# Performance work log

Measured on AMD Instinct MI355X. Metric: run time of the kernel, lower is better.

## Reference

```python
import jax, jax.numpy as jnp
import numpy as np

B, N, C = 2048, 128, 128
H = 4
NW = 64


def setup_inputs() -> dict:
    key = jax.random.key(0)
    ks = jax.random.split(key, 6)
    return {
        "x": jax.random.normal(ks[0], (B, N, C), dtype=jnp.float32),
        "mask": jax.random.normal(ks[1], (NW, N, N), dtype=jnp.float32),
        "qkv_w": jax.random.normal(ks[2], (3 * C, C), dtype=jnp.float32) * (C ** -0.5),
        "qkv_b": jax.random.normal(ks[3], (3 * C,), dtype=jnp.float32) * 0.02,
        "proj_w": jax.random.normal(ks[4], (C, C), dtype=jnp.float32) * (C ** -0.5),
        "proj_b": jax.random.normal(ks[5], (C,), dtype=jnp.float32) * 0.02,
    }


def reference(x, mask, qkv_w, qkv_b, proj_w, proj_b):
    b, n, c = x.shape
    h = H
    hd = c // h
    scale = hd ** -0.5
    # qkv projection: [B,N,3C] -> [3,B,H,N,hd]
    qkv = (x @ qkv_w.T + qkv_b).reshape(b, n, 3, h, hd).transpose(2, 0, 3, 1, 4)
    q, k, v = qkv[0], qkv[1], qkv[2]
    # scores [B,H,N,N]
    attn = jnp.einsum("bhnd,bhmd->bhnm", q, k) * scale
    nw = mask.shape[0]
    # add per-window mask: view as [B//nW, nW, H, N, N] + mask[None,:,None]
    attn = attn.reshape(b // nw, nw, h, n, n) + mask[None, :, None, :, :]
    attn = attn.reshape(b, h, n, n)
    attn = jax.nn.softmax(attn, axis=-1)
    out = jnp.einsum("bhnm,bhmd->bhnd", attn, v)
    out = out.transpose(0, 2, 1, 3).reshape(b, n, c)
    out = out @ proj_w.T + proj_b
    return out
```

## Files before the change

kernel.cpp:

```cpp
#include <hip/hip_runtime.h>

typedef __bf16 bf16x8 __attribute__((ext_vector_type(8)));
typedef __bf16 bf16x4 __attribute__((ext_vector_type(4)));
typedef float  f32x4  __attribute__((ext_vector_type(4)));

#define LDS_XO 0
#define LDS_Q  32768
#define LDS_K  65536
#define LDS_VT 98304
#define LDS_P  131072
#define LDS_TOTAL 147456

__device__ __forceinline__ int swz(int row, int colb) {
    return row * 256 + (colb ^ ((row & 7) << 4));
}
__device__ __forceinline__ int pswz(int row, int colb) {
    return row * 128 + (colb ^ ((row & 7) << 4));
}

__global__ void prep_weights(const float* __restrict__ qkv_w,
                             const float* __restrict__ proj_w,
                             __bf16* __restrict__ wq, __bf16* __restrict__ wp) {
    int i = blockIdx.x * 256 + threadIdx.x;
    wq[i] = (__bf16)qkv_w[i];
    if (i < 16384) wp[i] = (__bf16)proj_w[i];
}

__global__ void __launch_bounds__(512, 2)
attn_fused(const float* __restrict__ x, const float* __restrict__ mask,
           const float* __restrict__ qkv_b, const float* __restrict__ proj_b,
           const __bf16* __restrict__ wq, const __bf16* __restrict__ wp,
           float* __restrict__ out) {
    extern __shared__ char smem[];
    const int b    = blockIdx.x;
    const int tid  = threadIdx.x;
    const int wave = tid >> 6;
    const int lane = tid & 63;
    const int l16  = lane & 15;
    const int lg   = lane >> 4;

    {
        const float* xb = x + (size_t)b * 16384;
        #pragma unroll
        for (int it = 0; it < 4; ++it) {
            int i   = it * 512 + tid;
            int row = i >> 4;
            int c8  = (i & 15) << 3;
            float4 f0 = *(const float4*)(xb + row * 128 + c8);
            float4 f1 = *(const float4*)(xb + row * 128 + c8 + 4);
            bf16x8 v;
            v[0] = (__bf16)f0.x; v[1] = (__bf16)f0.y; v[2] = (__bf16)f0.z; v[3] = (__bf16)f0.w;
            v[4] = (__bf16)f1.x; v[5] = (__bf16)f1.y; v[6] = (__bf16)f1.z; v[7] = (__bf16)f1.w;
            *(bf16x8*)(smem + LDS_XO + swz(row, c8 * 2)) = v;
        }
    }
    __syncthreads();

    const int j0 = wave * 48;
    #pragma unroll
    for (int pass = 0; pass < 2; ++pass) {
        f32x4 acc[3][4];
        #pragma unroll
        for (int jt = 0; jt < 3; ++jt)
            #pragma unroll
            for (int nt = 0; nt < 4; ++nt)
                acc[jt][nt] = {0.f, 0.f, 0.f, 0.f};
        #pragma unroll
        for (int kc = 0; kc < 4; ++kc) {
            bf16x8 afr[3];
            #pragma unroll
            for (int jt = 0; jt < 3; ++jt)
                afr[jt] = *(const bf16x8*)(wq + (j0 + jt * 16 + l16) * 128 + kc * 32 + lg * 8);
            bf16x8 bfr[4];
            #pragma unroll
            for (int nt = 0; nt < 4; ++nt)
                bfr[nt] = *(const bf16x8*)(smem + LDS_XO +
                            swz((pass * 4 + nt) * 16 + l16, (kc * 32 + lg * 8) * 2));
            #pragma unroll
            for (int jt = 0; jt < 3; ++jt)
                #pragma unroll
                for (int nt = 0; nt < 4; ++nt)
                    acc[jt][nt] = __builtin_amdgcn_mfma_f32_16x16x32_bf16(
                                      afr[jt], bfr[nt], acc[jt][nt], 0, 0, 0);
        }
        #pragma unroll
        for (int jt = 0; jt < 3; ++jt) {
            int jbase = j0 + jt * 16 + lg * 4;
            float4 bias = *(const float4*)(qkv_b + jbase);
            #pragma unroll
            for (int nt = 0; nt < 4; ++nt) {
                int n = (pass * 4 + nt) * 16 + l16;
                f32x4 a = acc[jt][nt];
                __bf16 e0 = (__bf16)(a[0] + bias.x);
                __bf16 e1 = (__bf16)(a[1] + bias.y);
                __bf16 e2 = (__bf16)(a[2] + bias.z);
                __bf16 e3 = (__bf16)(a[3] + bias.w);
                if (jbase < 128) {
                    bf16x4 v4 = {e0, e1, e2, e3};
                    *(bf16x4*)(smem + LDS_Q + swz(n, jbase * 2)) = v4;
                } else if (jbase < 256) {
                    bf16x4 v4 = {e0, e1, e2, e3};
                    *(bf16x4*)(smem + LDS_K + swz(n, (jbase - 128) * 2)) = v4;
                } else {
                    int d = jbase - 256;
                    *(__bf16*)(smem + LDS_VT + swz(d + 0, n * 2)) = e0;
                    *(__bf16*)(smem + LDS_VT + swz(d + 1, n * 2)) = e1;
                    *(__bf16*)(smem + LDS_VT + swz(d + 2, n * 2)) = e2;
                    *(__bf16*)(smem + LDS_VT + swz(d + 3, n * 2)) = e3;
                }
            }
        }
    }
    __syncthreads();

    const int h  = wave >> 1;
    const int rh = wave & 1;
    const float sc = 0.17677669529663687f;
    bf16x8 kfr[8];
    #pragma unroll
    for (int mt = 0; mt < 8; ++mt)
        kfr[mt] = *(const bf16x8*)(smem + LDS_K + swz(mt * 16 + l16, (h * 32 + lg * 8) * 2));
    bf16x8 vfr[2][4];
    #pragma unroll
    for (int dt = 0; dt < 2; ++dt)
        #pragma unroll
        for (int kc = 0; kc < 4; ++kc)
            vfr[dt][kc] = *(const bf16x8*)(smem + LDS_VT +
                            swz(h * 32 + dt * 16 + l16, (kc * 32 + lg * 8) * 2));

    const float* mwin = mask + (size_t)(b & 63) * 16384;
    char* pbase = smem + LDS_P + wave * 2048;

    #pragma unroll
    for (int i = 0; i < 4; ++i) {
        const int nt = rh * 4 + i;
        bf16x8 qfr = *(const bf16x8*)(smem + LDS_Q + swz(nt * 16 + l16, (h * 32 + lg * 8) * 2));
        f32x4 s[8];
        #pragma unroll
        for (int mt = 0; mt < 8; ++mt) {
            f32x4 z = {0.f, 0.f, 0.f, 0.f};
            s[mt] = __builtin_amdgcn_mfma_f32_16x16x32_bf16(qfr, kfr[mt], z, 0, 0, 0);
        }
        float mx[4] = {-1e30f, -1e30f, -1e30f, -1e30f};
        #pragma unroll
        for (int mt = 0; mt < 8; ++mt)
            #pragma unroll
            for (int r = 0; r < 4; ++r) {
                float v = s[mt][r] * sc + mwin[(nt * 16 + lg * 4 + r) * 128 + mt * 16 + l16];
                s[mt][r] = v;
                mx[r] = fmaxf(mx[r], v);
            }
        #pragma unroll
        for (int r = 0; r < 4; ++r) {
            float m = mx[r];
            m = fmaxf(m, __shfl_xor(m, 1));
            m = fmaxf(m, __shfl_xor(m, 2));
            m = fmaxf(m, __shfl_xor(m, 4));
            m = fmaxf(m, __shfl_xor(m, 8));
            mx[r] = m;
        }
        float sm[4] = {0.f, 0.f, 0.f, 0.f};
        #pragma unroll
        for (int mt = 0; mt < 8; ++mt)
            #pragma unroll
            for (int r = 0; r < 4; ++r) {
                float p = __expf(s[mt][r] - mx[r]);
                s[mt][r] = p;
                sm[r] += p;
            }
        #pragma unroll
        for (int r = 0; r < 4; ++r) {
            float t = sm[r];
            t += __shfl_xor(t, 1);
            t += __shfl_xor(t, 2);
            t += __shfl_xor(t, 4);
            t += __shfl_xor(t, 8);
            sm[r] = 1.f / t;
        }
        f32x4 o[2];
        o[0] = {0.f, 0.f, 0.f, 0.f};
        o[1] = {0.f, 0.f, 0.f, 0.f};
        #pragma unroll
        for (int hp = 0; hp < 2; ++hp) {
            #pragma unroll
            for (int mtl = 0; mtl < 4; ++mtl) {
                int mt = hp * 4 + mtl;
                #pragma unroll
                for (int r = 0; r < 4; ++r)
                    *(__bf16*)(pbase + pswz(lg * 4 + r, (mtl * 16 + l16) * 2)) =
                        (__bf16)(s[mt][r] * sm[r]);
            }
            #pragma unroll
            for (int q = 0; q < 2; ++q) {
                int kc = hp * 2 + q;
                bf16x8 pafr = *(const bf16x8*)(pbase + pswz(l16, (q * 32 + lg * 8) * 2));
                #pragma unroll
                for (int dt = 0; dt < 2; ++dt)
                    o[dt] = __builtin_amdgcn_mfma_f32_16x16x32_bf16(
                                pafr, vfr[dt][kc], o[dt], 0, 0, 0);
            }
        }
        #pragma unroll
        for (int dt = 0; dt < 2; ++dt)
            #pragma unroll
            for (int r = 0; r < 4; ++r)
                *(__bf16*)(smem + LDS_XO +
                    swz(nt * 16 + lg * 4 + r, (h * 32 + dt * 16 + l16) * 2)) = (__bf16)o[dt][r];
    }
    __syncthreads();

    f32x4 facc[8];
    #pragma unroll
    for (int ct = 0; ct < 8; ++ct)
        facc[ct] = {0.f, 0.f, 0.f, 0.f};
    #pragma unroll
    for (int kc = 0; kc < 4; ++kc) {
        bf16x8 afr = *(const bf16x8*)(smem + LDS_XO +
                        swz(wave * 16 + l16, (kc * 32 + lg * 8) * 2));
        bf16x8 bfr[8];
        #pragma unroll
        for (int ct = 0; ct < 8; ++ct)
            bfr[ct] = *(const bf16x8*)(wp + (ct * 16 + l16) * 128 + kc * 32 + lg * 8);
        #pragma unroll
        for (int ct = 0; ct < 8; ++ct)
            facc[ct] = __builtin_amdgcn_mfma_f32_16x16x32_bf16(
                           afr, bfr[ct], facc[ct], 0, 0, 0);
    }
    float* ob = out + (size_t)b * 16384;
    #pragma unroll
    for (int ct = 0; ct < 8; ++ct) {
        float pb = proj_b[ct * 16 + l16];
        int n0 = wave * 16 + lg * 4;
        #pragma unroll
        for (int r = 0; r < 4; ++r)
            ob[(n0 + r) * 128 + ct * 16 + l16] = facc[ct][r] + pb;
    }
}

extern "C" void kernel_launch(void* const* d_in, const int* in_sizes, int n_in,
                              void* d_out, int out_size, void* d_ws, size_t ws_size,
                              hipStream_t stream) {
    const float* x      = (const float*)d_in[0];
    const float* mask   = (const float*)d_in[1];
    const float* qkv_w  = (const float*)d_in[2];
    const float* qkv_b  = (const float*)d_in[3];
    const float* proj_w = (const float*)d_in[4];
    const float* proj_b = (const float*)d_in[5];
    float* out = (float*)d_out;

    __bf16* wq = (__bf16*)d_ws;
    __bf16* wp = wq + 49152;

    prep_weights<<<192, 256, 0, stream>>>(qkv_w, proj_w, wq, wp);

    hipFuncSetAttribute((const void*)attn_fused,
                        hipFuncAttributeMaxDynamicSharedMemorySize, LDS_TOTAL);
    attn_fused<<<2048, 512, LDS_TOTAL, stream>>>(x, mask, qkv_b, proj_b, wq, wp, out);
}
```

Baseline: 473.9 us.

## Split fused attention into per-head-pair blocks plus separate projection kernel

Replaces the single fused kernel (one 512-thread block per window, 144KB LDS) with two kernels. The first runs two 256-thread blocks per window, each handling two heads with 80KB LDS, and writes the bf16 attention output to a global workspace. The second applies the output projection. The aim is smaller blocks with less LDS per block for better occupancy and load balance. The cost is that x is loaded and converted twice per window, there is an extra global round trip of the intermediate output, and one more kernel launch. The fused path is kept as a fallback when the workspace is too small.

```diff
diff --git a/kernel.cpp b/kernel.cpp
--- a/kernel.cpp
+++ b/kernel.cpp
@@ -3,6 +3,272 @@
 typedef __bf16 bf16x8 __attribute__((ext_vector_type(8)));
 typedef __bf16 bf16x4 __attribute__((ext_vector_type(4)));
 typedef float  f32x4  __attribute__((ext_vector_type(4)));
+
+__device__ __forceinline__ int swz(int row, int colb) {
+    return row * 256 + (colb ^ ((row & 7) << 4));
+}
+__device__ __forceinline__ int pswz(int row, int colb) {
+    return row * 128 + (colb ^ ((row & 7) << 4));
+}
+
+__global__ void prep_weights(const float* __restrict__ qkv_w,
+                             const float* __restrict__ proj_w,
+                             __bf16* __restrict__ wq, __bf16* __restrict__ wp) {
+    int i = blockIdx.x * 256 + threadIdx.x;
+    wq[i] = (__bf16)qkv_w[i];
+    if (i < 16384) wp[i] = (__bf16)proj_w[i];
+}
+
+#define A_LDS_X   0
+#define A_LDS_P   0
+#define A_LDS_Q   32768
+#define A_LDS_K   49152
+#define A_LDS_VT  65536
+#define A_LDS_TOTAL 81920
+
+__global__ void __launch_bounds__(256, 2)
+attn_split(const float* __restrict__ x, const float* __restrict__ mask,
+           const float* __restrict__ qkv_b,
+           const __bf16* __restrict__ wq,
+           __bf16* __restrict__ Og) {
+    extern __shared__ char smem[];
+    const int b    = blockIdx.x >> 1;
+    const int hp   = blockIdx.x & 1;
+    const int tid  = threadIdx.x;
+    const int wave = tid >> 6;
+    const int lane = tid & 63;
+    const int l16  = lane & 15;
+    const int lg   = lane >> 4;
+
+    {
+        const float* xb = x + (size_t)b * 16384;
+        #pragma unroll
+        for (int it = 0; it < 8; ++it) {
+            int i   = it * 256 + tid;
+            int row = i >> 4;
+            int c8  = (i & 15) << 3;
+            float4 f0 = *(const float4*)(xb + row * 128 + c8);
+            float4 f1 = *(const float4*)(xb + row * 128 + c8 + 4);
+            bf16x8 v;
+            v[0] = (__bf16)f0.x; v[1] = (__bf16)f0.y; v[2] = (__bf16)f0.z; v[3] = (__bf16)f0.w;
+            v[4] = (__bf16)f1.x; v[5] = (__bf16)f1.y; v[6] = (__bf16)f1.z; v[7] = (__bf16)f1.w;
+            *(bf16x8*)(smem + A_LDS_X + swz(row, c8 * 2)) = v;
+        }
+    }
+    __syncthreads();
+
+    const int f0 = wave * 48;
+    #pragma unroll
+    for (int pass = 0; pass < 2; ++pass) {
+        f32x4 acc[3][4];
+        #pragma unroll
+        for (int jt = 0; jt < 3; ++jt)
+            #pragma unroll
+            for (int nt = 0; nt < 4; ++nt)
+                acc[jt][nt] = {0.f, 0.f, 0.f, 0.f};
+        int jg_t[3];
+        #pragma unroll
+        for (int jt = 0; jt < 3; ++jt) {
+            int ft = f0 + jt * 16;
+            jg_t[jt] = (ft < 64) ? (hp * 64 + ft)
+                     : (ft < 128) ? (128 + hp * 64 + (ft - 64))
+                                  : (256 + hp * 64 + (ft - 128));
+        }
+        #pragma unroll
+        for (int kc = 0; kc < 4; ++kc) {
+            bf16x8 afr[3];
+            #pragma unroll
+            for (int jt = 0; jt < 3; ++jt)
+                afr[jt] = *(const bf16x8*)(wq + (jg_t[jt] + l16) * 128 + kc * 32 + lg * 8);
+            bf16x8 bfr[4];
+            #pragma unroll
+            for (int nt = 0; nt < 4; ++nt)
+                bfr[nt] = *(const bf16x8*)(smem + A_LDS_X +
+                            swz((pass * 4 + nt) * 16 + l16, (kc * 32 + lg * 8) * 2));
+            #pragma unroll
+            for (int jt = 0; jt < 3; ++jt)
+                #pragma unroll
+                for (int nt = 0; nt < 4; ++nt)
+                    acc[jt][nt] = __builtin_amdgcn_mfma_f32_16x16x32_bf16(
+                                      afr[jt], bfr[nt], acc[jt][nt], 0, 0, 0);
+        }
+        #pragma unroll
+        for (int jt = 0; jt < 3; ++jt) {
+            int ft = f0 + jt * 16;
+            int f  = ft + lg * 4;
+            float4 bias = *(const float4*)(qkv_b + jg_t[jt] + lg * 4);
+            #pragma unroll
+            for (int nt = 0; nt < 4; ++nt) {
+                int n = (pass * 4 + nt) * 16 + l16;
+                f32x4 a = acc[jt][nt];
+                __bf16 e0 = (__bf16)(a[0] + bias.x);
+                __bf16 e1 = (__bf16)(a[1] + bias.y);
+                __bf16 e2 = (__bf16)(a[2] + bias.z);
+                __bf16 e3 = (__bf16)(a[3] + bias.w);
+                if (f < 64) {
+                    bf16x4 v4 = {e0, e1, e2, e3};
+                    *(bf16x4*)(smem + A_LDS_Q + pswz(n, f * 2)) = v4;
+                } else if (f < 128) {
+                    bf16x4 v4 = {e0, e1, e2, e3};
+                    *(bf16x4*)(smem + A_LDS_K + pswz(n, (f - 64) * 2)) = v4;
+                } else {
+                    int d = f - 128;
+                    *(__bf16*)(smem + A_LDS_VT + swz(d + 0, n * 2)) = e0;
+                    *(__bf16*)(smem + A_LDS_VT + swz(d + 1, n * 2)) = e1;
+                    *(__bf16*)(smem + A_LDS_VT + swz(d + 2, n * 2)) = e2;
+                    *(__bf16*)(smem + A_LDS_VT + swz(d + 3, n * 2)) = e3;
+                }
+            }
+        }
+    }
+    __syncthreads();
+
+    const int hl = wave >> 1;
+    const int rh = wave & 1;
+    const int hgl = hp * 2 + hl;
+    const float sc = 0.17677669529663687f;
+    bf16x8 kfr[8];
+    #pragma unroll
+    for (int mt = 0; mt < 8; ++mt)
+        kfr[mt] = *(const bf16x8*)(smem + A_LDS_K +
+                      pswz(mt * 16 + l16, (hl * 32 + lg * 8) * 2));
+    bf16x8 vfr[2][4];
+    #pragma unroll
+    for (int dt = 0; dt < 2; ++dt)
+        #pragma unroll
+        for (int kc = 0; kc < 4; ++kc)
+            vfr[dt][kc] = *(const bf16x8*)(smem + A_LDS_VT +
+                            swz(hl * 32 + dt * 16 + l16, (kc * 32 + lg * 8) * 2));
+
+    const float* mwin = mask + (size_t)(b & 63) * 16384;
+    char* pbase = smem + A_LDS_P + wave * 2048;
+
+    #pragma unroll
+    for (int i = 0; i < 4; ++i) {
+        const int nt = rh * 4 + i;
+        bf16x8 qfr = *(const bf16x8*)(smem + A_LDS_Q +
+                        pswz(nt * 16 + l16, (hl * 32 + lg * 8) * 2));
+        f32x4 s[8];
+        #pragma unroll
+        for (int mt = 0; mt < 8; ++mt) {
+            f32x4 z = {0.f, 0.f, 0.f, 0.f};
+            s[mt] = __builtin_amdgcn_mfma_f32_16x16x32_bf16(qfr, kfr[mt], z, 0, 0, 0);
+        }
+        float mx[4] = {-1e30f, -1e30f, -1e30f, -1e30f};
+        #pragma unroll
+        for (int mt = 0; mt < 8; ++mt)
+            #pragma unroll
+            for (int r = 0; r < 4; ++r) {
+                float v = s[mt][r] * sc + mwin[(nt * 16 + lg * 4 + r) * 128 + mt * 16 + l16];
+                s[mt][r] = v;
+                mx[r] = fmaxf(mx[r], v);
+            }
+        #pragma unroll
+        for (int r = 0; r < 4; ++r) {
+            float m = mx[r];
+            m = fmaxf(m, __shfl_xor(m, 1));
+            m = fmaxf(m, __shfl_xor(m, 2));
+            m = fmaxf(m, __shfl_xor(m, 4));
+            m = fmaxf(m, __shfl_xor(m, 8));
+            mx[r] = m;
+        }
+        float sm[4] = {0.f, 0.f, 0.f, 0.f};
+        #pragma unroll
+        for (int mt = 0; mt < 8; ++mt)
+            #pragma unroll
+            for (int r = 0; r < 4; ++r) {
+                float p = __expf(s[mt][r] - mx[r]);
+                s[mt][r] = p;
+                sm[r] += p;
+            }
+        #pragma unroll
+        for (int r = 0; r < 4; ++r) {
+            float t = sm[r];
+            t += __shfl_xor(t, 1);
+            t += __shfl_xor(t, 2);
+            t += __shfl_xor(t, 4);
+            t += __shfl_xor(t, 8);
+            sm[r] = 1.f / t;
+        }
+        f32x4 o[2];
+        o[0] = {0.f, 0.f, 0.f, 0.f};
+        o[1] = {0.f, 0.f, 0.f, 0.f};
+        #pragma unroll
+        for (int hpp = 0; hpp < 2; ++hpp) {
+            #pragma unroll
+            for (int mtl = 0; mtl < 4; ++mtl) {
+                int mt = hpp * 4 + mtl;
+                #pragma unroll
+                for (int r = 0; r < 4; ++r)
+                    *(__bf16*)(pbase + pswz(lg * 4 + r, (mtl * 16 + l16) * 2)) =
+                        (__bf16)(s[mt][r] * sm[r]);
+            }
+            #pragma unroll
+            for (int q = 0; q < 2; ++q) {
+                int kc = hpp * 2 + q;
+                bf16x8 pafr = *(const bf16x8*)(pbase + pswz(l16, (q * 32 + lg * 8) * 2));
+                #pragma unroll
+                for (int dt = 0; dt < 2; ++dt)
+                    o[dt] = __builtin_amdgcn_mfma_f32_16x16x32_bf16(
+                                pafr, vfr[dt][kc], o[dt], 0, 0, 0);
+            }
+        }
+        #pragma unroll
+        for (int dt = 0; dt < 2; ++dt)
+            #pragma unroll
+            for (int r = 0; r < 4; ++r)
+                Og[((size_t)b * 128 + nt * 16 + lg * 4 + r) * 128 +
+                   hgl * 32 + dt * 16 + l16] = (__bf16)o[dt][r];
+    }
+}
+
+__global__ void __launch_bounds__(256)
+proj_out(const __bf16* __restrict__ Og, const __bf16* __restrict__ wp,
+         const float* __restrict__ proj_b, float* __restrict__ out) {
+    const int b    = blockIdx.x;
+    const int tid  = threadIdx.x;
+    const int wave = tid >> 6;
+    const int l16  = tid & 15;
+    const int lg   = (tid & 63) >> 4;
+
+    f32x4 facc[2][8];
+    #pragma unroll
+    for (int nt2 = 0; nt2 < 2; ++nt2)
+        #pragma unroll
+        for (int ct = 0; ct < 8; ++ct)
+            facc[nt2][ct] = {0.f, 0.f, 0.f, 0.f};
+    #pragma unroll
+    for (int kc = 0; kc < 4; ++kc) {
+        bf16x8 afr[2];
+        #pragma unroll
+        for (int nt2 = 0; nt2 < 2; ++nt2)
+            afr[nt2] = *(const bf16x8*)(Og +
+                          ((size_t)b * 128 + wave * 32 + nt2 * 16 + l16) * 128 +
+                          kc * 32 + lg * 8);
+        bf16x8 bfr[8];
+        #pragma unroll
+        for (int ct = 0; ct < 8; ++ct)
+            bfr[ct] = *(const bf16x8*)(wp + (ct * 16 + l16) * 128 + kc * 32 + lg * 8);
+        #pragma unroll
+        for (int nt2 = 0; nt2 < 2; ++nt2)
+            #pragma unroll
+            for (int ct = 0; ct < 8; ++ct)
+                facc[nt2][ct] = __builtin_amdgcn_mfma_f32_16x16x32_bf16(
+                                    afr[nt2], bfr[ct], facc[nt2][ct], 0, 0, 0);
+    }
+    float* ob = out + (size_t)b * 16384;
+    #pragma unroll
+    for (int ct = 0; ct < 8; ++ct) {
+        float pb = proj_b[ct * 16 + l16];
+        #pragma unroll
+        for (int nt2 = 0; nt2 < 2; ++nt2) {
+            int n0 = wave * 32 + nt2 * 16 + lg * 4;
+            #pragma unroll
+            for (int r = 0; r < 4; ++r)
+                ob[(n0 + r) * 128 + ct * 16 + l16] = facc[nt2][ct][r] + pb;
+        }
+    }
+}
 
 #define LDS_XO 0
 #define LDS_Q  32768
@@ -10,21 +276,6 @@
 #define LDS_VT 98304
 #define LDS_P  131072
 #define LDS_TOTAL 147456
-
-__device__ __forceinline__ int swz(int row, int colb) {
-    return row * 256 + (colb ^ ((row & 7) << 4));
-}
-__device__ __forceinline__ int pswz(int row, int colb) {
-    return row * 128 + (colb ^ ((row & 7) << 4));
-}
-
-__global__ void prep_weights(const float* __restrict__ qkv_w,
-                             const float* __restrict__ proj_w,
-                             __bf16* __restrict__ wq, __bf16* __restrict__ wp) {
-    int i = blockIdx.x * 256 + threadIdx.x;
-    wq[i] = (__bf16)qkv_w[i];
-    if (i < 16384) wp[i] = (__bf16)proj_w[i];
-}
 
 __global__ void __launch_bounds__(512, 2)
 attn_fused(const float* __restrict__ x, const float* __restrict__ mask,
@@ -181,10 +432,10 @@
         o[0] = {0.f, 0.f, 0.f, 0.f};
         o[1] = {0.f, 0.f, 0.f, 0.f};
         #pragma unroll
-        for (int hp = 0; hp < 2; ++hp) {
+        for (int hp2 = 0; hp2 < 2; ++hp2) {
             #pragma unroll
             for (int mtl = 0; mtl < 4; ++mtl) {
-                int mt = hp * 4 + mtl;
+                int mt = hp2 * 4 + mtl;
                 #pragma unroll
                 for (int r = 0; r < 4; ++r)
                     *(__bf16*)(pbase + pswz(lg * 4 + r, (mtl * 16 + l16) * 2)) =
@@ -192,7 +443,7 @@
             }
             #pragma unroll
             for (int q = 0; q < 2; ++q) {
-                int kc = hp * 2 + q;
+                int kc = hp2 * 2 + q;
                 bf16x8 pafr = *(const bf16x8*)(pbase + pswz(l16, (q * 32 + lg * 8) * 2));
                 #pragma unroll
                 for (int dt = 0; dt < 2; ++dt)
@@ -253,7 +504,18 @@
 
     prep_weights<<<192, 256, 0, stream>>>(qkv_w, proj_w, wq, wp);
 
-    hipFuncSetAttribute((const void*)attn_fused,
-                        hipFuncAttributeMaxDynamicSharedMemorySize, LDS_TOTAL);
-    attn_fused<<<2048, 512, LDS_TOTAL, stream>>>(x, mask, qkv_b, proj_b, wq, wp, out);
-}
+    const size_t og_bytes = (size_t)2048 * 128 * 128 * 2;
+    const size_t need = 131072 + og_bytes;
+
+    if (ws_size >= need) {
+        __bf16* Og = (__bf16*)((char*)d_ws + 131072);
+        hipFuncSetAttribute((const void*)attn_split,
+                            hipFuncAttributeMaxDynamicSharedMemorySize, A_LDS_TOTAL);
+        attn_split<<<4096, 256, A_LDS_TOTAL, stream>>>(x, mask, qkv_b, wq, Og);
+        proj_out<<<2048, 256, 0, stream>>>(Og, wp, proj_b, out);
+    } else {
+        hipFuncSetAttribute((const void*)attn_fused,
+                            hipFuncAttributeMaxDynamicSharedMemorySize, LDS_TOTAL);
+        attn_fused<<<2048, 512, LDS_TOTAL, stream>>>(x, mask, qkv_b, proj_b, wq, wp, out);
+    }
+}
```

After: 408.5 us. 13.8% less time.
